# Kernel tuning notes

Hardware: AMD Instinct MI355X
Metric: run time of the kernel (lower is better)

Reference implementation:

```python
import jax, jax.numpy as jnp
import numpy as np

HIDDEN = 1280
HEADS = 16
HEAD_DIM = HIDDEN // HEADS  # 80
TOTAL = 8192
N_CHUNKS = 8


def rotate_half(x):
    x1, x2 = jnp.split(x, 2, axis=-1)
    return jnp.concatenate([-x2, x1], axis=-1)


def setup_inputs() -> dict:
    key = jax.random.key(0)
    ks = jax.random.split(key, 7)
    hidden_states = jax.random.normal(ks[0], (TOTAL, HIDDEN), dtype=jnp.float32)
    cos = jax.random.uniform(ks[1], (TOTAL, HEAD_DIM), dtype=jnp.float32)
    sin = jax.random.uniform(ks[2], (TOTAL, HEAD_DIM), dtype=jnp.float32)
    s = 1.0 / np.sqrt(HIDDEN)
    w_qkv = jax.random.normal(ks[3], (HIDDEN, 3 * HIDDEN), dtype=jnp.float32) * s
    b_qkv = jax.random.normal(ks[4], (3 * HIDDEN,), dtype=jnp.float32) * 0.01
    w_proj = jax.random.normal(ks[5], (HIDDEN, HIDDEN), dtype=jnp.float32) * s
    b_proj = jax.random.normal(ks[6], (HIDDEN,), dtype=jnp.float32) * 0.01
    return {"hidden_states": hidden_states, "cos": cos, "sin": sin,
            "w_qkv": w_qkv, "b_qkv": b_qkv, "w_proj": w_proj,
            "b_proj": b_proj, "n_chunks": N_CHUNKS}


def reference(hidden_states, cos, sin, w_qkv, b_qkv, w_proj, b_proj, n_chunks):
    T, D = hidden_states.shape
    C = int(n_chunks)
    L = T // C  # equal-length chunks (block-diagonal varlen attention)
    H, hd = HEADS, HEAD_DIM
    scale = hd ** -0.5

    qkv = hidden_states @ w_qkv + b_qkv                    # [T, 3D]
    q, k, v = jnp.split(qkv, 3, axis=-1)
    # [C, L, H, hd]
    q = q.reshape(C, L, H, hd)
    k = k.reshape(C, L, H, hd)
    v = v.reshape(C, L, H, hd)
    cos_c = cos.reshape(C, L, 1, hd)
    sin_c = sin.reshape(C, L, 1, hd)
    q = q * cos_c + rotate_half(q) * sin_c
    k = k * cos_c + rotate_half(k) * sin_c

    # block-diagonal attention: each chunk attends only within itself
    scores = jnp.einsum('clhd,cmhd->chlm', q, k) * scale   # [C, H, L, L]
    weights = jax.nn.softmax(scores.astype(jnp.float32), axis=-1).astype(v.dtype)
    attn = jnp.einsum('chlm,cmhd->clhd', weights, v)       # [C, L, H, hd]
    attn = attn.reshape(T, D)
    return attn @ w_proj + b_proj
```

## Files before the change

### kernel.cpp

```cpp
#include <hip/hip_runtime.h>

#define T_TOK 8192
#define D_HID 1280
#define H_    16
#define HD_   80
#define C_    8
#define L_    1024
#define N3_   3840
#define QPAD  96

typedef _Float16 f16;
typedef __attribute__((ext_vector_type(8))) _Float16 h8;
typedef __attribute__((ext_vector_type(4))) float f32x4;

__global__ __launch_bounds__(256) void convert_x(const float* __restrict__ x,
                                                 f16* __restrict__ y) {
  const int g = blockIdx.x * 256 + threadIdx.x;
  const float4 v = ((const float4*)x)[g];
  f16 o[4] = {(f16)v.x, (f16)v.y, (f16)v.z, (f16)v.w};
  ((uint2*)y)[g] = *(const uint2*)o;
}

__global__ __launch_bounds__(256) void convert_w_t(const float* __restrict__ W,
                                                   f16* __restrict__ Wt,
                                                   int K, int N) {
  __shared__ float tile[32][33];
  const int n0 = blockIdx.x * 32, k0 = blockIdx.y * 32;
  const int c = threadIdx.x & 31, r0 = threadIdx.x >> 5;
#pragma unroll
  for (int it = 0; it < 4; ++it) {
    const int r = r0 + it * 8;
    tile[r][c] = W[(size_t)(k0 + r) * N + n0 + c];
  }
  __syncthreads();
#pragma unroll
  for (int it = 0; it < 4; ++it) {
    const int r = r0 + it * 8;
    Wt[(size_t)(n0 + r) * K + k0 + c] = (f16)tile[c][r];
  }
}

__device__ __forceinline__ void stage_rows512(const f16* __restrict__ gbase, int K,
                                              f16* sdst, int tid) {
#pragma unroll
  for (int s0 = 0; s0 < 2048; s0 += 512) {
    const int s = s0 + tid;
    const int row = s >> 3;
    const int part = (s & 7) ^ (row & 7);
    const f16* gp = gbase + (size_t)row * K + part * 8;
    __builtin_amdgcn_global_load_lds(
        (const __attribute__((address_space(1))) void*)gp,
        (__attribute__((address_space(3))) void*)(sdst + s * 8),
        16, 0, 0);
  }
}

__device__ __forceinline__ h8 fragld64(const f16* s, int row, int c) {
  const int slot = c ^ (row & 7);
  return *(const h8*)&s[row * 64 + slot * 8];
}

__global__ __launch_bounds__(512, 2) void gemm_f16(
    const f16* __restrict__ A, const f16* __restrict__ B,
    const float* __restrict__ bias,
    float* __restrict__ Cf, f16* __restrict__ Ch,
    int M, int N, int K) {
  __shared__ f16 sAB[2][2][256 * 64];
  const int tid = threadIdx.x;
  const int wave = tid >> 6, lane = tid & 63;
  const int quad = lane >> 4, ln = lane & 15;

  const int nwg = gridDim.x;
  int wg = blockIdx.x;
  wg = (wg & 7) * (nwg >> 3) + (wg >> 3);
  const int nbx = N >> 8;
  const int bm = (wg / nbx) * 256, bn = (wg % nbx) * 256;
  const int wm = (wave >> 2) * 128, wn = (wave & 3) * 64;

  f32x4 acc[8][4];
#pragma unroll
  for (int i = 0; i < 8; ++i)
#pragma unroll
    for (int j = 0; j < 4; ++j) acc[i][j] = (f32x4){0.f, 0.f, 0.f, 0.f};

  const f16* Abase = A + (size_t)bm * K;
  const f16* Bbase = B + (size_t)bn * K;

  stage_rows512(Abase, K, sAB[0][0], tid);
  stage_rows512(Bbase, K, sAB[0][1], tid);

  const int nt = K >> 6;
  for (int t = 0; t < nt; ++t) {
    if (t + 1 < nt) {
      stage_rows512(Abase + (t + 1) * 64, K, sAB[(t + 1) & 1][0], tid);
      stage_rows512(Bbase + (t + 1) * 64, K, sAB[(t + 1) & 1][1], tid);
      asm volatile("s_waitcnt vmcnt(8)" ::: "memory");
    } else {
      asm volatile("s_waitcnt vmcnt(0)" ::: "memory");
    }
    __builtin_amdgcn_sched_barrier(0);
    __builtin_amdgcn_s_barrier();

    const f16* sA = sAB[t & 1][0];
    const f16* sB = sAB[t & 1][1];
#pragma unroll
    for (int ks = 0; ks < 2; ++ks) {
      h8 af[8], bf[4];
#pragma unroll
      for (int i = 0; i < 8; ++i) af[i] = fragld64(sA, wm + i * 16 + ln, ks * 4 + quad);
#pragma unroll
      for (int j = 0; j < 4; ++j) bf[j] = fragld64(sB, wn + j * 16 + ln, ks * 4 + quad);
      __builtin_amdgcn_s_setprio(1);
#pragma unroll
      for (int i = 0; i < 8; ++i)
#pragma unroll
        for (int j = 0; j < 4; ++j)
          acc[i][j] = __builtin_amdgcn_mfma_f32_16x16x32_f16(af[i], bf[j], acc[i][j], 0, 0, 0);
      __builtin_amdgcn_s_setprio(0);
    }
    __builtin_amdgcn_s_barrier();
  }

  float bv[4];
#pragma unroll
  for (int j = 0; j < 4; ++j) bv[j] = bias[bn + wn + j * 16 + ln];
#pragma unroll
  for (int i = 0; i < 8; ++i)
#pragma unroll
    for (int j = 0; j < 4; ++j)
#pragma unroll
      for (int r = 0; r < 4; ++r) {
        const int row = bm + wm + i * 16 + quad * 4 + r;
        const int col = bn + wn + j * 16 + ln;
        const float val = acc[i][j][r] + bv[j];
        if (Ch) Ch[(size_t)row * N + col] = (f16)val;
        else    Cf[(size_t)row * N + col] = val;
      }
}

__global__ __launch_bounds__(256) void rope_convert(
    const f16* __restrict__ qkv, const float* __restrict__ cosb,
    const float* __restrict__ sinb, f16* __restrict__ Qb, f16* __restrict__ Kb) {
  const int tid = threadIdx.x;
  const int wave = tid >> 6, lane = tid & 63;
  const int t = blockIdx.x * 4 + wave;
  const size_t rowb = (size_t)t * N3_;
  const float qscale = 0.11180339887498949f;
#pragma unroll
  for (int u = 0; u < 5; ++u) {
    const int g = u * 64 + lane;
    const int e = g * 8;
    const int d = e % HD_;
    const int h = (e % D_HID) / HD_;
    const bool isK = e >= D_HID;
    const bool lo = d < 40;
    const int pe = lo ? e + 40 : e - 40;
    f16 v[8], p[8];
    *(int4*)v = *(const int4*)(qkv + rowb + e);
    *(int4*)p = *(const int4*)(qkv + rowb + pe);
    const float4 cs0 = *(const float4*)(cosb + (size_t)t * HD_ + d);
    const float4 cs1 = *(const float4*)(cosb + (size_t)t * HD_ + d + 4);
    const float4 sn0 = *(const float4*)(sinb + (size_t)t * HD_ + d);
    const float4 sn1 = *(const float4*)(sinb + (size_t)t * HD_ + d + 4);
    const float cs[8] = {cs0.x, cs0.y, cs0.z, cs0.w, cs1.x, cs1.y, cs1.z, cs1.w};
    const float sn[8] = {sn0.x, sn0.y, sn0.z, sn0.w, sn1.x, sn1.y, sn1.z, sn1.w};
    f16 o[8];
#pragma unroll
    for (int j = 0; j < 8; ++j) {
      const float pv = lo ? -(float)p[j] : (float)p[j];
      const float ov = (float)v[j] * cs[j] + pv * sn[j];
      o[j] = (f16)(isK ? ov : ov * qscale);
    }
    *(int4*)((isK ? Kb : Qb) + ((size_t)h * T_TOK + t) * QPAD + d) = *(const int4*)o;
  }
  {
    const int qk = lane >> 5, h = (lane >> 1) & 15, half = lane & 1;
    f16* dst = (qk ? Kb : Qb) + ((size_t)h * T_TOK + t) * QPAD + 80 + half * 8;
    *(int4*)dst = make_int4(0, 0, 0, 0);
  }
}

__global__ __launch_bounds__(256) void vt_convert(const f16* __restrict__ qkv,
                                                  f16* __restrict__ Vt) {
  __shared__ f16 tl[HD_][136];
  const int h = blockIdx.x & 15;
  const int t0 = (blockIdx.x >> 4) * 128;
  const int tid = threadIdx.x;
#pragma unroll
  for (int it = 0; it < 5; ++it) {
    const int e = tid + it * 256;
    const int t = e / 10, pc = e % 10;
    int4 v = *(const int4*)(qkv + (size_t)(t0 + t) * N3_ + 2 * D_HID + h * HD_ + pc * 8);
    f16 tmp[8];
    *(int4*)tmp = v;
#pragma unroll
    for (int u = 0; u < 8; ++u) tl[pc * 8 + u][t] = tmp[u];
  }
  __syncthreads();
#pragma unroll
  for (int it = 0; it < 5; ++it) {
    const int e = tid + it * 256;
    const int d = e >> 4, pt = e & 15;
    *(int4*)(Vt + ((size_t)h * HD_ + d) * T_TOK + t0 + pt * 8) = *(const int4*)&tl[d][pt * 8];
  }
}

__global__ __launch_bounds__(256, 2) void attn_flash(
    const f16* __restrict__ Qb, const f16* __restrict__ Kb,
    const f16* __restrict__ Vt, f16* __restrict__ Oa) {
  __shared__ f16 Ps[4][64][72];
  const int tid = threadIdx.x;
  const int wave = tid >> 6, lane = tid & 63;
  const int quad = lane >> 4, ln = lane & 15;
  const int h = blockIdx.x & 15;
  const int qb = (blockIdx.x >> 4) & 3;
  const int c = blockIdx.x >> 6;
  const int t0 = c * L_ + qb * 256 + wave * 64;
  const size_t hb = (size_t)h * T_TOK;

  h8 aq[4][3];
#pragma unroll
  for (int i = 0; i < 4; ++i)
#pragma unroll
    for (int ks = 0; ks < 3; ++ks)
      aq[i][ks] = *(const h8*)(Qb + (hb + t0 + i * 16 + ln) * QPAD + ks * 32 + quad * 8);

  f32x4 o[4][5];
  float lsum[4][4];
#pragma unroll
  for (int i = 0; i < 4; ++i) {
#pragma unroll
    for (int jn = 0; jn < 5; ++jn) o[i][jn] = (f32x4){0.f, 0.f, 0.f, 0.f};
#pragma unroll
    for (int r = 0; r < 4; ++r) lsum[i][r] = 0.f;
  }

  for (int kb = 0; kb < 16; ++kb) {
    const int kt0 = c * L_ + kb * 64;
#pragma unroll
    for (int j = 0; j < 4; ++j) {
      h8 bk[3];
#pragma unroll
      for (int ks = 0; ks < 3; ++ks)
        bk[ks] = *(const h8*)(Kb + (hb + kt0 + j * 16 + ln) * QPAD + ks * 32 + quad * 8);
      f32x4 s[4];
#pragma unroll
      for (int i = 0; i < 4; ++i) s[i] = (f32x4){0.f, 0.f, 0.f, 0.f};
      __builtin_amdgcn_s_setprio(1);
#pragma unroll
      for (int ks = 0; ks < 3; ++ks)
#pragma unroll
        for (int i = 0; i < 4; ++i)
          s[i] = __builtin_amdgcn_mfma_f32_16x16x32_f16(aq[i][ks], bk[ks], s[i], 0, 0, 0);
      __builtin_amdgcn_s_setprio(0);
#pragma unroll
      for (int i = 0; i < 4; ++i)
#pragma unroll
        for (int r = 0; r < 4; ++r) {
          const float p = __expf(s[i][r]);
          lsum[i][r] += p;
          Ps[wave][i * 16 + quad * 4 + r][j * 16 + ln] = (f16)p;
        }
    }
#pragma unroll
    for (int ks = 0; ks < 2; ++ks) {
      h8 ap[4];
#pragma unroll
      for (int i = 0; i < 4; ++i)
        ap[i] = *(const h8*)&Ps[wave][i * 16 + ln][ks * 32 + quad * 8];
#pragma unroll
      for (int jn = 0; jn < 5; ++jn) {
        const h8 bv = *(const h8*)(Vt + ((size_t)h * HD_ + jn * 16 + ln) * T_TOK
                                   + kt0 + ks * 32 + quad * 8);
        __builtin_amdgcn_s_setprio(1);
#pragma unroll
        for (int i = 0; i < 4; ++i)
          o[i][jn] = __builtin_amdgcn_mfma_f32_16x16x32_f16(ap[i], bv, o[i][jn], 0, 0, 0);
        __builtin_amdgcn_s_setprio(0);
      }
    }
  }

#pragma unroll
  for (int i = 0; i < 4; ++i)
#pragma unroll
    for (int r = 0; r < 4; ++r) {
      float s = lsum[i][r];
#pragma unroll
      for (int off = 1; off < 16; off <<= 1) s += __shfl_xor(s, off);
      lsum[i][r] = 1.f / s;
    }

#pragma unroll
  for (int i = 0; i < 4; ++i)
#pragma unroll
    for (int r = 0; r < 4; ++r) {
      const int t = t0 + i * 16 + quad * 4 + r;
      const float inv = lsum[i][r];
#pragma unroll
      for (int jn = 0; jn < 5; ++jn)
        Oa[(size_t)t * D_HID + h * HD_ + jn * 16 + ln] = (f16)(o[i][jn][r] * inv);
    }
}

extern "C" void kernel_launch(void* const* d_in, const int* in_sizes, int n_in,
                              void* d_out, int out_size, void* d_ws, size_t ws_size,
                              hipStream_t stream) {
  (void)in_sizes; (void)n_in; (void)out_size; (void)ws_size;
  const float* x      = (const float*)d_in[0];
  const float* cosb   = (const float*)d_in[1];
  const float* sinb   = (const float*)d_in[2];
  const float* w_qkv  = (const float*)d_in[3];
  const float* b_qkv  = (const float*)d_in[4];
  const float* w_proj = (const float*)d_in[5];
  const float* b_proj = (const float*)d_in[6];
  float* out = (float*)d_out;

  char* ws = (char*)d_ws;
  f16* qkv_h  = (f16*)(ws);
  f16* attn_h = (f16*)(ws);
  f16* x_h    = (f16*)(ws + 62914560);
  f16* Qb     = (f16*)(ws + 62914560);
  f16* Kb     = (f16*)(ws + 88080384);
  f16* Vt     = (f16*)(ws + 113246208);
  f16* wq_t   = (f16*)(ws + 134217728);
  f16* wp_t   = (f16*)(ws + 144048128);

  convert_x<<<(T_TOK * D_HID / 4) / 256, 256, 0, stream>>>(x, x_h);
  convert_w_t<<<dim3(N3_ / 32, D_HID / 32), 256, 0, stream>>>(w_qkv, wq_t, D_HID, N3_);
  convert_w_t<<<dim3(D_HID / 32, D_HID / 32), 256, 0, stream>>>(w_proj, wp_t, D_HID, D_HID);
  gemm_f16<<<(N3_ / 256) * (T_TOK / 256), 512, 0, stream>>>(
      x_h, wq_t, b_qkv, nullptr, qkv_h, T_TOK, N3_, D_HID);
  rope_convert<<<T_TOK / 4, 256, 0, stream>>>(qkv_h, cosb, sinb, Qb, Kb);
  vt_convert<<<H_ * (T_TOK / 128), 256, 0, stream>>>(qkv_h, Vt);
  attn_flash<<<C_ * 4 * H_, 256, 0, stream>>>(Qb, Kb, Vt, attn_h);
  gemm_f16<<<(D_HID / 256) * (T_TOK / 256), 512, 0, stream>>>(
      attn_h, wp_t, b_proj, out, nullptr, T_TOK, D_HID, D_HID);
}
```

Measured before the change: 375.8 us.

## Restructure GEMM main loop into four quadrant phases with interleaved half-tile staging

Splits each K-iteration of the f16 GEMM into four MFMA quadrant phases. Each phase loads only the fragments it needs and issues half-tile global-to-LDS loads between the phases. The B tile for the next step and the A tile two steps ahead are prefetched, with finer vmcnt waits and extra barriers. This aims to overlap memory traffic with matrix-core work and reduce register pressure from holding all fragments at once. The cost is more barriers per iteration and more intricate buffer-reuse ordering.

```diff
diff --git a/kernel.cpp b/kernel.cpp
--- a/kernel.cpp
+++ b/kernel.cpp
@@ -40,17 +40,17 @@
   }
 }
 
-__device__ __forceinline__ void stage_rows512(const f16* __restrict__ gbase, int K,
-                                              f16* sdst, int tid) {
-#pragma unroll
-  for (int s0 = 0; s0 < 2048; s0 += 512) {
-    const int s = s0 + tid;
-    const int row = s >> 3;
+__device__ __forceinline__ void stage_half(const f16* __restrict__ gpanel, int K,
+                                           f16* sdst, int t, int half) {
+#pragma unroll
+  for (int r = 0; r < 2; ++r) {
+    const int s = r * 512 + (int)threadIdx.x;
+    const int row = half * 128 + (s >> 3);
     const int part = (s & 7) ^ (row & 7);
-    const f16* gp = gbase + (size_t)row * K + part * 8;
+    const f16* gp = gpanel + (size_t)row * K + t * 64 + part * 8;
     __builtin_amdgcn_global_load_lds(
         (const __attribute__((address_space(1))) void*)gp,
-        (__attribute__((address_space(3))) void*)(sdst + s * 8),
+        (__attribute__((address_space(3))) void*)(sdst + row * 64 + (s & 7) * 8),
         16, 0, 0);
   }
 }
@@ -85,40 +85,101 @@
 
   const f16* Abase = A + (size_t)bm * K;
   const f16* Bbase = B + (size_t)bn * K;
-
-  stage_rows512(Abase, K, sAB[0][0], tid);
-  stage_rows512(Bbase, K, sAB[0][1], tid);
-
   const int nt = K >> 6;
+
+  stage_half(Abase, K, sAB[0][0], 0, 0);
+  stage_half(Abase, K, sAB[0][0], 0, 1);
+  stage_half(Bbase, K, sAB[0][1], 0, 0);
+  stage_half(Bbase, K, sAB[0][1], 0, 1);
+  stage_half(Abase, K, sAB[1][0], 1, 0);
+  stage_half(Abase, K, sAB[1][0], 1, 1);
+  asm volatile("s_waitcnt vmcnt(4)" ::: "memory");
+  __builtin_amdgcn_sched_barrier(0);
+  __builtin_amdgcn_s_barrier();
+
   for (int t = 0; t < nt; ++t) {
-    if (t + 1 < nt) {
-      stage_rows512(Abase + (t + 1) * 64, K, sAB[(t + 1) & 1][0], tid);
-      stage_rows512(Bbase + (t + 1) * 64, K, sAB[(t + 1) & 1][1], tid);
-      asm volatile("s_waitcnt vmcnt(8)" ::: "memory");
-    } else {
-      asm volatile("s_waitcnt vmcnt(0)" ::: "memory");
-    }
-    __builtin_amdgcn_sched_barrier(0);
-    __builtin_amdgcn_s_barrier();
-
     const f16* sA = sAB[t & 1][0];
     const f16* sB = sAB[t & 1][1];
-#pragma unroll
-    for (int ks = 0; ks < 2; ++ks) {
-      h8 af[8], bf[4];
-#pragma unroll
-      for (int i = 0; i < 8; ++i) af[i] = fragld64(sA, wm + i * 16 + ln, ks * 4 + quad);
-#pragma unroll
-      for (int j = 0; j < 4; ++j) bf[j] = fragld64(sB, wn + j * 16 + ln, ks * 4 + quad);
-      __builtin_amdgcn_s_setprio(1);
-#pragma unroll
-      for (int i = 0; i < 8; ++i)
-#pragma unroll
-        for (int j = 0; j < 4; ++j)
-          acc[i][j] = __builtin_amdgcn_mfma_f32_16x16x32_f16(af[i], bf[j], acc[i][j], 0, 0, 0);
-      __builtin_amdgcn_s_setprio(0);
-    }
-    __builtin_amdgcn_s_barrier();
+    const int nb = (t + 1) & 1;
+    h8 af[4][2], bf01[2][2], bf23[2][2];
+
+#pragma unroll
+    for (int i = 0; i < 4; ++i)
+#pragma unroll
+      for (int ks = 0; ks < 2; ++ks)
+        af[i][ks] = fragld64(sA, wm + i * 16 + ln, ks * 4 + quad);
+#pragma unroll
+    for (int j = 0; j < 2; ++j)
+#pragma unroll
+      for (int ks = 0; ks < 2; ++ks)
+        bf01[j][ks] = fragld64(sB, wn + j * 16 + ln, ks * 4 + quad);
+    if (t + 1 < nt) stage_half(Bbase, K, sAB[nb][1], t + 1, 0);
+    __builtin_amdgcn_s_barrier();
+    __builtin_amdgcn_s_setprio(1);
+#pragma unroll
+    for (int ks = 0; ks < 2; ++ks)
+#pragma unroll
+      for (int i = 0; i < 4; ++i)
+#pragma unroll
+        for (int j = 0; j < 2; ++j)
+          acc[i][j] = __builtin_amdgcn_mfma_f32_16x16x32_f16(af[i][ks], bf01[j][ks], acc[i][j], 0, 0, 0);
+    __builtin_amdgcn_s_setprio(0);
+    __builtin_amdgcn_s_barrier();
+
+#pragma unroll
+    for (int j = 0; j < 2; ++j)
+#pragma unroll
+      for (int ks = 0; ks < 2; ++ks)
+        bf23[j][ks] = fragld64(sB, wn + (j + 2) * 16 + ln, ks * 4 + quad);
+    if (t + 1 < nt) stage_half(Bbase, K, sAB[nb][1], t + 1, 1);
+    __builtin_amdgcn_s_barrier();
+    __builtin_amdgcn_s_setprio(1);
+#pragma unroll
+    for (int ks = 0; ks < 2; ++ks)
+#pragma unroll
+      for (int i = 0; i < 4; ++i)
+#pragma unroll
+        for (int j = 0; j < 2; ++j)
+          acc[i][j + 2] = __builtin_amdgcn_mfma_f32_16x16x32_f16(af[i][ks], bf23[j][ks], acc[i][j + 2], 0, 0, 0);
+    __builtin_amdgcn_s_setprio(0);
+    __builtin_amdgcn_s_barrier();
+
+#pragma unroll
+    for (int i = 0; i < 4; ++i)
+#pragma unroll
+      for (int ks = 0; ks < 2; ++ks)
+        af[i][ks] = fragld64(sA, wm + (i + 4) * 16 + ln, ks * 4 + quad);
+    __builtin_amdgcn_s_barrier();
+    __builtin_amdgcn_s_setprio(1);
+#pragma unroll
+    for (int ks = 0; ks < 2; ++ks)
+#pragma unroll
+      for (int i = 0; i < 4; ++i)
+#pragma unroll
+        for (int j = 0; j < 2; ++j)
+          acc[i + 4][j + 2] = __builtin_amdgcn_mfma_f32_16x16x32_f16(af[i][ks], bf23[j][ks], acc[i + 4][j + 2], 0, 0, 0);
+    __builtin_amdgcn_s_setprio(0);
+    __builtin_amdgcn_s_barrier();
+
+    if (t + 2 < nt) {
+      stage_half(Abase, K, sAB[t & 1][0], t + 2, 0);
+      stage_half(Abase, K, sAB[t & 1][0], t + 2, 1);
+    }
+    __builtin_amdgcn_s_setprio(1);
+#pragma unroll
+    for (int ks = 0; ks < 2; ++ks)
+#pragma unroll
+      for (int i = 0; i < 4; ++i)
+#pragma unroll
+        for (int j = 0; j < 2; ++j)
+          acc[i + 4][j] = __builtin_amdgcn_mfma_f32_16x16x32_f16(af[i][ks], bf01[j][ks], acc[i + 4][j], 0, 0, 0);
+    __builtin_amdgcn_s_setprio(0);
+    if (t + 1 < nt) {
+      if (t + 2 < nt) asm volatile("s_waitcnt vmcnt(4)" ::: "memory");
+      else            asm volatile("s_waitcnt vmcnt(0)" ::: "memory");
+      __builtin_amdgcn_sched_barrier(0);
+      __builtin_amdgcn_s_barrier();
+    }
   }
 
   float bv[4];
```

Result: no change. 370.0 us (-1.5%).
